# Kernel tuning notes

Measured on AMD Instinct MI355X. Metric: run time of the kernel, lower is better.

The kernel has to match this reference:

```python
import jax, jax.numpy as jnp
import numpy as np

K = 1024
H = 16
HEAD = K // H

def setup_inputs() -> dict:
    key = jax.random.key(0)
    ks = jax.random.split(key, 6)
    b, t = 2, 2048
    x = jax.random.normal(ks[0], (b, t, K), dtype=jnp.float32)
    padding = jnp.ones((b, t), dtype=jnp.int32)
    s = 1.0 / np.sqrt(K)
    Wq = jax.random.normal(ks[1], (K, K), dtype=jnp.float32) * s
    Wk = jax.random.normal(ks[2], (K, K), dtype=jnp.float32) * s
    Wv = jax.random.normal(ks[3], (K, K), dtype=jnp.float32) * s
    Wo = jax.random.normal(ks[4], (K, K), dtype=jnp.float32) * s
    bo = jnp.zeros((K,), dtype=jnp.float32)
    return {"x": x, "padding": padding, "Wq": Wq, "Wk": Wk, "Wv": Wv, "Wo": Wo, "bo": bo}

def reference(x, padding, Wq, Wk, Wv, Wo, bo):
    b, t, k = x.shape
    h, d = H, HEAD
    # projections (nn.Linear: x @ W.T), then split heads -> [b,h,t,d]
    q = (x @ Wq.T).reshape(b, t, h, d).transpose(0, 2, 1, 3)
    kk = (x @ Wk.T).reshape(b, t, h, d).transpose(0, 2, 1, 3)
    v = (x @ Wv.T).reshape(b, t, h, d).transpose(0, 2, 1, 3)
    scores = jnp.einsum('bhqd,bhkd->bhqk', q, kk)
    # key-side padding mask: positions with padding==0 get -inf (before scaling,
    # same result since -inf/sqrt(d) == -inf)
    mask = (padding == 0)[:, None, None, :]  # [b,1,1,t]
    scores = jnp.where(mask, -jnp.inf, scores) / np.sqrt(d).astype(np.float32)
    weights = jax.nn.softmax(scores, axis=-1)
    out = jnp.einsum('bhqk,bhkd->bhqd', weights, v)
    out = out.transpose(0, 2, 1, 3).reshape(b, t, h * d)
    return out @ Wo.T + bo
```

## Files before the change

kernel.cpp:

```cpp
#include <hip/hip_runtime.h>
#include <cmath>
#include <stdint.h>

#define K_DIM 1024
#define NH    16
#define HD    64
#define T     2048
#define NTOK  4096
#define NBH   32

typedef __bf16 bf16x8 __attribute__((ext_vector_type(8)));
typedef float  f32x4  __attribute__((ext_vector_type(4)));

__device__ __forceinline__ unsigned short f2bf(float f) {
  union { float f; unsigned u; } v; v.f = f;
  unsigned u = v.u;
  return (unsigned short)((u + 0x7FFFu + ((u >> 16) & 1u)) >> 16);
}
__device__ __forceinline__ unsigned short f2bf_hu(float f) {
  union { float f; unsigned u; } v; v.f = f;
  return (unsigned short)((v.u + 0x8000u) >> 16);
}

__device__ __forceinline__ void gload16(const void* g, void* l) {
  __builtin_amdgcn_global_load_lds(
      (__attribute__((address_space(1))) void*)(g),
      (__attribute__((address_space(3))) void*)(l),
      16, 0, 0);
}

__global__ void convert_kernel(const float* __restrict__ x,
                               const float* __restrict__ Wq,
                               const float* __restrict__ Wk,
                               const float* __restrict__ Wv,
                               const float* __restrict__ Wo,
                               unsigned short* __restrict__ xb,
                               unsigned short* __restrict__ wqkv,
                               unsigned short* __restrict__ wob)
{
  const size_t NX = (size_t)NTOK * K_DIM;
  const size_t NW = (size_t)K_DIM * K_DIM;
  size_t i = ((size_t)blockIdx.x * blockDim.x + threadIdx.x) * 4;
  const float* src; unsigned short* dst; size_t off;
  if (i < NX)             { src = x;  dst = xb;          off = i; }
  else if (i < NX + NW)   { src = Wq; dst = wqkv;        off = i - NX; }
  else if (i < NX + 2*NW) { src = Wk; dst = wqkv + NW;   off = i - NX - NW; }
  else if (i < NX + 3*NW) { src = Wv; dst = wqkv + 2*NW; off = i - NX - 2*NW; }
  else                    { src = Wo; dst = wob;         off = i - NX - 3*NW; }
  float4 v = *(const float4*)(src + off);
  ushort4 o;
  o.x = f2bf(v.x); o.y = f2bf(v.y); o.z = f2bf(v.z); o.w = f2bf(v.w);
  *(ushort4*)(dst + off) = o;
}

template <int MODE, int TM, int TN>
__global__ __launch_bounds__(256, 2)
void gemm_bt(const unsigned short* __restrict__ A,
             const unsigned short* __restrict__ B,
             unsigned short* __restrict__ o_q,
             unsigned short* __restrict__ o_k,
             unsigned short* __restrict__ o_v,
             float* __restrict__ o_f,
             const float* __restrict__ bias)
{
  __shared__ unsigned short Asm[TM * 64];
  __shared__ unsigned short Bsm[TN * 64];
  const int tid  = threadIdx.x;
  const int wave = tid >> 6;
  const int lane = tid & 63;
  const int lq   = lane & 15;
  const int quad = lane >> 4;
  const int bm = blockIdx.x, bn = blockIdx.y;
  const int wm = (wave >> 1) * (TM / 2), wn = (wave & 1) * (TN / 2);
  const int MT = TM / 32, NT = TN / 32;

  f32x4 acc[MT][NT];
#pragma unroll
  for (int i = 0; i < MT; ++i)
#pragma unroll
    for (int j = 0; j < NT; ++j) acc[i][j] = (f32x4){0.f, 0.f, 0.f, 0.f};

  const char* Ab = (const char*)(A + (size_t)bm * TM * K_DIM);
  const char* Bb = (const char*)(B + (size_t)bn * TN * K_DIM);

  for (int k0 = 0; k0 < K_DIM; k0 += 64) {
#pragma unroll
    for (int i = 0; i < MT; ++i) {
      int off   = i * 4096 + wave * 1024 + lane * 16;
      int row   = off >> 7;
      int chunk = (off >> 4) & 7;
      int scol  = (chunk ^ (row & 7)) << 4;
      gload16(Ab + (size_t)row * (K_DIM * 2) + (size_t)k0 * 2 + scol,
              (char*)Asm + off - lane * 16);
    }
#pragma unroll
    for (int i = 0; i < NT; ++i) {
      int off   = i * 4096 + wave * 1024 + lane * 16;
      int row   = off >> 7;
      int chunk = (off >> 4) & 7;
      int scol  = (chunk ^ (row & 7)) << 4;
      gload16(Bb + (size_t)row * (K_DIM * 2) + (size_t)k0 * 2 + scol,
              (char*)Bsm + off - lane * 16);
    }
    __syncthreads();
#pragma unroll
    for (int kk = 0; kk < 64; kk += 32) {
      bf16x8 af[MT], bfr[NT];
#pragma unroll
      for (int mt = 0; mt < MT; ++mt) {
        int row = wm + mt * 16 + lq;
        int sw  = (quad + (kk >> 3)) ^ (row & 7);
        af[mt] = *(const bf16x8*)((const char*)Asm + row * 128 + (sw << 4));
      }
#pragma unroll
      for (int nt = 0; nt < NT; ++nt) {
        int row = wn + nt * 16 + lq;
        int sw  = (quad + (kk >> 3)) ^ (row & 7);
        bfr[nt] = *(const bf16x8*)((const char*)Bsm + row * 128 + (sw << 4));
      }
#pragma unroll
      for (int mt = 0; mt < MT; ++mt)
#pragma unroll
        for (int nt = 0; nt < NT; ++nt)
          acc[mt][nt] = __builtin_amdgcn_mfma_f32_16x16x32_bf16(af[mt], bfr[nt], acc[mt][nt], 0, 0, 0);
    }
    __syncthreads();
  }

#pragma unroll
  for (int mt = 0; mt < MT; ++mt) {
#pragma unroll
    for (int r = 0; r < 4; ++r) {
      int m = bm * TM + wm + mt * 16 + quad * 4 + r;
#pragma unroll
      for (int nt = 0; nt < NT; ++nt) {
        int n = bn * TN + wn + nt * 16 + lq;
        float v = acc[mt][nt][r];
        if (MODE == 0) {
          int b = m >> 11, t = m & 2047;
          int which = n >> 10, c = n & 1023;
          int h = c >> 6, d = c & 63;
          if (which == 0)
            o_q[((size_t)(b * NH + h) * T + t) * HD + d] = f2bf(v);
          else if (which == 1)
            o_k[((size_t)(b * NH + h) * T + t) * HD + d] = f2bf(v);
          else
            o_v[((size_t)(b * NH + h) * HD + d) * T + t] = f2bf(v);
        } else {
          o_f[(size_t)m * K_DIM + n] = v + bias[n];
        }
      }
    }
  }
}

__global__ __launch_bounds__(256, 2)
void attn_kernel(const unsigned short* __restrict__ Q,
                 const unsigned short* __restrict__ Kb,
                 const unsigned short* __restrict__ Vt,
                 const int* __restrict__ padding,
                 unsigned short* __restrict__ O)
{
  __shared__ unsigned short Ksm[128 * 64];
  __shared__ unsigned short Vsm[64 * 128];
  __shared__ unsigned short Psm[8][16 * 128];

  const int tid  = threadIdx.x;
  const int wave = tid >> 6;
  const int lane = tid & 63;
  const int lq   = lane & 15;
  const int quad = lane >> 4;
  const int qt = blockIdx.x;
  const int bh = blockIdx.y;
  const int b  = bh >> 4;
  const int h  = bh & 15;
  const int qbase = qt * 128 + wave * 32;

  bf16x8 qf[2][2];
#pragma unroll
  for (int mt = 0; mt < 2; ++mt)
#pragma unroll
    for (int kk = 0; kk < 2; ++kk)
      qf[mt][kk] = *(const bf16x8*)&Q[((size_t)bh * T + qbase + mt * 16 + lq) * HD + kk * 32 + quad * 8];

  f32x4 o_acc[2][4];
  f32x4 l_part[2];
#pragma unroll
  for (int mt = 0; mt < 2; ++mt) {
    l_part[mt] = (f32x4){0.f, 0.f, 0.f, 0.f};
#pragma unroll
    for (int i = 0; i < 4; ++i) o_acc[mt][i] = (f32x4){0.f, 0.f, 0.f, 0.f};
  }

  const float Cs = 0.18033688011112042f;

  for (int kt = 0; kt < T / 128; ++kt) {
#pragma unroll
    for (int i = 0; i < 4; ++i) {
      int off = i * 4096 + wave * 1024 + lane * 16;
      {
        int row = off >> 7, chunk = (off >> 4) & 7;
        int scol = (chunk ^ (row & 7)) << 4;
        gload16((const char*)Kb + ((size_t)(bh * T + kt * 128 + row) * HD) * 2 + scol,
                (char*)Ksm + off - lane * 16);
      }
      {
        int row = off >> 8, chunk = (off >> 4) & 15;
        int scol = (chunk ^ (row & 15)) << 4;
        gload16((const char*)Vt + ((size_t)(bh * HD + row) * T + (size_t)kt * 128) * 2 + scol,
                (char*)Vsm + off - lane * 16);
      }
    }

    float biasb[8];
#pragma unroll
    for (int nt = 0; nt < 8; ++nt)
      biasb[nt] = (padding[b * T + kt * 128 + nt * 16 + lq] == 0) ? -INFINITY : 0.f;

    __syncthreads();

    f32x4 s[2][8];
#pragma unroll
    for (int mt = 0; mt < 2; ++mt)
#pragma unroll
      for (int nt = 0; nt < 8; ++nt) s[mt][nt] = (f32x4){0.f, 0.f, 0.f, 0.f};
#pragma unroll
    for (int kk = 0; kk < 2; ++kk) {
#pragma unroll
      for (int nt = 0; nt < 8; ++nt) {
        int row = nt * 16 + lq;
        int sw  = (quad + kk * 4) ^ (row & 7);
        bf16x8 kf = *(const bf16x8*)((const char*)Ksm + row * 128 + (sw << 4));
        s[0][nt] = __builtin_amdgcn_mfma_f32_16x16x32_bf16(qf[0][kk], kf, s[0][nt], 0, 0, 0);
        s[1][nt] = __builtin_amdgcn_mfma_f32_16x16x32_bf16(qf[1][kk], kf, s[1][nt], 0, 0, 0);
      }
    }

#pragma unroll
    for (int mt = 0; mt < 2; ++mt) {
#pragma unroll
      for (int nt = 0; nt < 8; ++nt) {
#pragma unroll
        for (int r = 0; r < 4; ++r) {
          float p = __builtin_amdgcn_exp2f(s[mt][nt][r] * Cs + biasb[nt]);
          s[mt][nt][r] = p;
          l_part[mt][r] += p;
        }
      }
    }

#pragma unroll
    for (int mt = 0; mt < 2; ++mt) {
      char* pbase = (char*)&Psm[wave * 2 + mt][0];
#pragma unroll
      for (int r = 0; r < 4; ++r) {
        int row = quad * 4 + r;
#pragma unroll
        for (int nt = 0; nt < 8; ++nt) {
          int colb = (nt * 16 + lq) * 2;
          *(unsigned short*)(pbase + row * 256 + (colb ^ (row << 4))) = f2bf_hu(s[mt][nt][r]);
        }
      }
    }
    asm volatile("s_waitcnt lgkmcnt(0)" ::: "memory");

#pragma unroll
    for (int kk = 0; kk < 4; ++kk) {
      int swp = ((kk * 4 + quad) ^ lq) << 4;
      bf16x8 pf0 = *(const bf16x8*)((const char*)&Psm[wave * 2 + 0][0] + lq * 256 + swp);
      bf16x8 pf1 = *(const bf16x8*)((const char*)&Psm[wave * 2 + 1][0] + lq * 256 + swp);
#pragma unroll
      for (int dt = 0; dt < 4; ++dt) {
        int row = dt * 16 + lq;
        int sw  = ((kk * 4 + quad) ^ (row & 15)) << 4;
        bf16x8 vf = *(const bf16x8*)((const char*)Vsm + row * 256 + sw);
        o_acc[0][dt] = __builtin_amdgcn_mfma_f32_16x16x32_bf16(pf0, vf, o_acc[0][dt], 0, 0, 0);
        o_acc[1][dt] = __builtin_amdgcn_mfma_f32_16x16x32_bf16(pf1, vf, o_acc[1][dt], 0, 0, 0);
      }
    }
    __syncthreads();
  }

#pragma unroll
  for (int mt = 0; mt < 2; ++mt) {
#pragma unroll
    for (int r = 0; r < 4; ++r) {
      float lsum = l_part[mt][r];
#pragma unroll
      for (int x = 1; x < 16; x <<= 1) lsum += __shfl_xor(lsum, x);
      float inv = (lsum > 0.f) ? 1.f / lsum : 0.f;
      int t = qbase + mt * 16 + quad * 4 + r;
#pragma unroll
      for (int dt = 0; dt < 4; ++dt) {
        int chan = h * HD + dt * 16 + lq;
        O[((size_t)(b * T + t)) * K_DIM + chan] = f2bf(o_acc[mt][dt][r] * inv);
      }
    }
  }
}

extern "C" void kernel_launch(void* const* d_in, const int* in_sizes, int n_in,
                              void* d_out, int out_size, void* d_ws, size_t ws_size,
                              hipStream_t stream)
{
  const float* x       = (const float*)d_in[0];
  const int*   padding = (const int*)d_in[1];
  const float* Wq      = (const float*)d_in[2];
  const float* Wk      = (const float*)d_in[3];
  const float* Wv      = (const float*)d_in[4];
  const float* Wo      = (const float*)d_in[5];
  const float* bo      = (const float*)d_in[6];
  float* out = (float*)d_out;

  char* ws = (char*)d_ws;
  unsigned short* xb   = (unsigned short*)(ws);
  unsigned short* wqkv = (unsigned short*)(ws + (8u  << 20));
  unsigned short* wob  = (unsigned short*)(ws + (14u << 20));
  unsigned short* qb   = (unsigned short*)(ws + (16u << 20));
  unsigned short* kb   = (unsigned short*)(ws + (24u << 20));
  unsigned short* vtb  = (unsigned short*)(ws + (32u << 20));
  unsigned short* ab   = (unsigned short*)(ws + (40u << 20));

  convert_kernel<<<8192, 256, 0, stream>>>(x, Wq, Wk, Wv, Wo, xb, wqkv, wob);

  gemm_bt<0, 128, 128><<<dim3(32, 24), 256, 0, stream>>>(xb, wqkv, qb, kb, vtb, nullptr, nullptr);

  attn_kernel<<<dim3(16, 32), 256, 0, stream>>>(qb, kb, vtb, padding, ab);

  gemm_bt<2, 64, 128><<<dim3(64, 8), 256, 0, stream>>>(ab, wob, nullptr, nullptr, nullptr, out, bo);
}
```

Before: 195.6 us.

## Swap GEMM operands for vectorized epilogue stores and halve attention P buffer

The GEMM epilogues are restructured so each lane writes four contiguous outputs as one vector store. To get that, Q/K projection and the output projection are computed transposed (weights as the A operand), and V gets its own GEMM that writes the transposed layout. The attention kernel stages P through shared memory in two 64-column halves, which halves the P buffer and raises the occupancy target from 2 to 3 blocks. The cost is an extra kernel launch, an extra LDS wait per half, and a dependence on the grid and index remapping being correct.

```diff
diff --git a/kernel.cpp b/kernel.cpp
--- a/kernel.cpp
+++ b/kernel.cpp
@@ -129,32 +129,38 @@
 
 #pragma unroll
   for (int mt = 0; mt < MT; ++mt) {
-#pragma unroll
-    for (int r = 0; r < 4; ++r) {
-      int m = bm * TM + wm + mt * 16 + quad * 4 + r;
-#pragma unroll
-      for (int nt = 0; nt < NT; ++nt) {
-        int n = bn * TN + wn + nt * 16 + lq;
-        float v = acc[mt][nt][r];
-        if (MODE == 0) {
-          int b = m >> 11, t = m & 2047;
-          int which = n >> 10, c = n & 1023;
-          int h = c >> 6, d = c & 63;
-          if (which == 0)
-            o_q[((size_t)(b * NH + h) * T + t) * HD + d] = f2bf(v);
-          else if (which == 1)
-            o_k[((size_t)(b * NH + h) * T + t) * HD + d] = f2bf(v);
-          else
-            o_v[((size_t)(b * NH + h) * HD + d) * T + t] = f2bf(v);
-        } else {
-          o_f[(size_t)m * K_DIM + n] = v + bias[n];
-        }
-      }
-    }
-  }
-}
-
-__global__ __launch_bounds__(256, 2)
+    int mbase = bm * TM + wm + mt * 16 + quad * 4;
+#pragma unroll
+    for (int nt = 0; nt < NT; ++nt) {
+      int n = bn * TN + wn + nt * 16 + lq;
+      if (MODE == 1) {
+        int which = mbase >> 10, c = mbase & 1023;
+        int h = c >> 6, d0 = c & 63;
+        int b = n >> 11, t = n & 2047;
+        ushort4 pk;
+        pk.x = f2bf(acc[mt][nt][0]); pk.y = f2bf(acc[mt][nt][1]);
+        pk.z = f2bf(acc[mt][nt][2]); pk.w = f2bf(acc[mt][nt][3]);
+        unsigned short* dst = which ? o_k : o_q;
+        *(ushort4*)&dst[((size_t)(b * NH + h) * T + t) * HD + d0] = pk;
+      } else if (MODE == 0) {
+        int b = mbase >> 11, t0 = mbase & 2047;
+        int h = n >> 6, d = n & 63;
+        ushort4 pk;
+        pk.x = f2bf(acc[mt][nt][0]); pk.y = f2bf(acc[mt][nt][1]);
+        pk.z = f2bf(acc[mt][nt][2]); pk.w = f2bf(acc[mt][nt][3]);
+        *(ushort4*)&o_v[((size_t)(b * NH + h) * HD + d) * T + t0] = pk;
+      } else {
+        float4 bv = *(const float4*)&bias[mbase];
+        float4 o;
+        o.x = acc[mt][nt][0] + bv.x; o.y = acc[mt][nt][1] + bv.y;
+        o.z = acc[mt][nt][2] + bv.z; o.w = acc[mt][nt][3] + bv.w;
+        *(float4*)&o_f[(size_t)n * K_DIM + mbase] = o;
+      }
+    }
+  }
+}
+
+__global__ __launch_bounds__(256, 3)
 void attn_kernel(const unsigned short* __restrict__ Q,
                  const unsigned short* __restrict__ Kb,
                  const unsigned short* __restrict__ Vt,
@@ -163,7 +169,7 @@
 {
   __shared__ unsigned short Ksm[128 * 64];
   __shared__ unsigned short Vsm[64 * 128];
-  __shared__ unsigned short Psm[8][16 * 128];
+  __shared__ unsigned short Psm[8][16 * 64];
 
   const int tid  = threadIdx.x;
   const int wave = tid >> 6;
@@ -250,33 +256,38 @@
     }
 
 #pragma unroll
-    for (int mt = 0; mt < 2; ++mt) {
-      char* pbase = (char*)&Psm[wave * 2 + mt][0];
-#pragma unroll
-      for (int r = 0; r < 4; ++r) {
-        int row = quad * 4 + r;
-#pragma unroll
-        for (int nt = 0; nt < 8; ++nt) {
-          int colb = (nt * 16 + lq) * 2;
-          *(unsigned short*)(pbase + row * 256 + (colb ^ (row << 4))) = f2bf_hu(s[mt][nt][r]);
+    for (int half = 0; half < 2; ++half) {
+#pragma unroll
+      for (int mt = 0; mt < 2; ++mt) {
+        char* pbase = (char*)&Psm[wave * 2 + mt][0];
+#pragma unroll
+        for (int r = 0; r < 4; ++r) {
+          int row = quad * 4 + r;
+#pragma unroll
+          for (int nt = 0; nt < 4; ++nt) {
+            int colb = (nt * 16 + lq) * 2;
+            *(unsigned short*)(pbase + row * 128 + (colb ^ ((row & 7) << 4))) =
+                f2bf_hu(s[mt][half * 4 + nt][r]);
+          }
         }
       }
-    }
-    asm volatile("s_waitcnt lgkmcnt(0)" ::: "memory");
-
-#pragma unroll
-    for (int kk = 0; kk < 4; ++kk) {
-      int swp = ((kk * 4 + quad) ^ lq) << 4;
-      bf16x8 pf0 = *(const bf16x8*)((const char*)&Psm[wave * 2 + 0][0] + lq * 256 + swp);
-      bf16x8 pf1 = *(const bf16x8*)((const char*)&Psm[wave * 2 + 1][0] + lq * 256 + swp);
-#pragma unroll
-      for (int dt = 0; dt < 4; ++dt) {
-        int row = dt * 16 + lq;
-        int sw  = ((kk * 4 + quad) ^ (row & 15)) << 4;
-        bf16x8 vf = *(const bf16x8*)((const char*)Vsm + row * 256 + sw);
-        o_acc[0][dt] = __builtin_amdgcn_mfma_f32_16x16x32_bf16(pf0, vf, o_acc[0][dt], 0, 0, 0);
-        o_acc[1][dt] = __builtin_amdgcn_mfma_f32_16x16x32_bf16(pf1, vf, o_acc[1][dt], 0, 0, 0);
-      }
+      asm volatile("s_waitcnt lgkmcnt(0)" ::: "memory");
+
+#pragma unroll
+      for (int kk2 = 0; kk2 < 2; ++kk2) {
+        int swp = (((kk2 * 4 + quad) ^ (lq & 7)) << 4);
+        bf16x8 pf0 = *(const bf16x8*)((const char*)&Psm[wave * 2 + 0][0] + lq * 128 + swp);
+        bf16x8 pf1 = *(const bf16x8*)((const char*)&Psm[wave * 2 + 1][0] + lq * 128 + swp);
+#pragma unroll
+        for (int dt = 0; dt < 4; ++dt) {
+          int row = dt * 16 + lq;
+          int sw  = ((half * 8 + kk2 * 4 + quad) ^ lq) << 4;
+          bf16x8 vf = *(const bf16x8*)((const char*)Vsm + row * 256 + sw);
+          o_acc[0][dt] = __builtin_amdgcn_mfma_f32_16x16x32_bf16(pf0, vf, o_acc[0][dt], 0, 0, 0);
+          o_acc[1][dt] = __builtin_amdgcn_mfma_f32_16x16x32_bf16(pf1, vf, o_acc[1][dt], 0, 0, 0);
+        }
+      }
+      asm volatile("s_waitcnt lgkmcnt(0)" ::: "memory");
     }
     __syncthreads();
   }
@@ -323,9 +334,11 @@
 
   convert_kernel<<<8192, 256, 0, stream>>>(x, Wq, Wk, Wv, Wo, xb, wqkv, wob);
 
-  gemm_bt<0, 128, 128><<<dim3(32, 24), 256, 0, stream>>>(xb, wqkv, qb, kb, vtb, nullptr, nullptr);
+  gemm_bt<1, 128, 128><<<dim3(16, 32), 256, 0, stream>>>(wqkv, xb, qb, kb, nullptr, nullptr, nullptr);
+
+  gemm_bt<0, 128, 64><<<dim3(32, 16), 256, 0, stream>>>(xb, wqkv + 2u * K_DIM * K_DIM, nullptr, nullptr, vtb, nullptr, nullptr);
 
   attn_kernel<<<dim3(16, 32), 256, 0, stream>>>(qb, kb, vtb, padding, ab);
 
-  gemm_bt<2, 64, 128><<<dim3(64, 8), 256, 0, stream>>>(ab, wob, nullptr, nullptr, nullptr, out, bo);
-}
+  gemm_bt<2, 64, 128><<<dim3(16, 32), 256, 0, stream>>>(wob, ab, nullptr, nullptr, nullptr, out, bo);
+}
```

Measured after the change: 248.9 us. 27.3% more time.
